# Optimization experiments

Measured on AMD Instinct MI355X. Metric: run time of the kernel, lower is better.

The kernel has to match this reference:

```python
import jax, jax.numpy as jnp
import numpy as np

B, N, C, K = 8, 4096, 128, 16
EPS = 1e-5  # BatchNorm1d default eps


def setup_inputs() -> dict:
    key = jax.random.key(0)
    k0, k1, k2 = jax.random.split(key, 3)
    xyz = jax.random.normal(k0, (B, N, 3), jnp.float32)
    x = jax.random.normal(k1, (B, C, N), jnp.float32)
    # Conv1d(channel, channel, kernel_size=1, bias=False) weight -> [C_out, C_in]
    W = jax.random.normal(k2, (C, C), jnp.float32) / np.sqrt(C)
    gamma = jnp.ones((C,), jnp.float32)
    beta = jnp.zeros((C,), jnp.float32)
    running_mean = jnp.zeros((C,), jnp.float32)
    running_var = jnp.ones((C,), jnp.float32)
    return {"xyz": xyz, "x": x, "W": W, "gamma": gamma, "beta": beta,
            "running_mean": running_mean, "running_var": running_var}


def _knn_idx(xyz, k):
    # squared pairwise distances d2[b,i,j] = ||xyz[b,i]-xyz[b,j]||^2
    s = jnp.sum(xyz * xyz, axis=-1)                      # [B,N]
    d2 = s[:, :, None] + s[:, None, :] - 2.0 * jnp.einsum('bnd,bmd->bnm', xyz, xyz)
    # keops argKmin over dim=1; d2 is symmetric so top_k over the last axis is equivalent
    _, idx = jax.lax.top_k(-d2, k)                       # [B,N,K]
    return idx


def reference(xyz, x, W, gamma, beta, running_mean, running_var):
    idx = _knn_idx(xyz, K)                               # [B,N,K] int32
    x_t = jnp.transpose(x, (0, 2, 1))                    # [B,N,C]
    grouped = jax.vmap(lambda pts, i: pts[i])(x_t, idx)  # [B,N,K,C] gather
    g = jnp.transpose(grouped, (0, 3, 2, 1))             # [B,C,K,N]
    # 1x1 Conv1d (no bias): GEMM over channel dim
    y = jnp.einsum('oc,bckn->bokn', W, g)                # [B,C,K,N]
    # BatchNorm1d (inference form with running stats)
    scale = gamma * jax.lax.rsqrt(running_var + EPS)     # [C]
    y = y * scale[None, :, None, None] + (beta - running_mean * scale)[None, :, None, None]
    y = jax.nn.relu(y)
    return jnp.max(y, axis=2)                            # max over k neighbors -> [B,C,N]
```

## Files before the change

kernel.cpp:

```cpp
#include <hip/hip_runtime.h>
#include <hip/hip_bf16.h>

#define BATCH 8
#define NPTS  4096
#define CCH   128
#define KNN_K 16

typedef __attribute__((ext_vector_type(8))) short  bf16x8;
typedef __attribute__((ext_vector_type(4))) float  f32x4;


static __device__ __forceinline__ short f2bf(float v) {
    __hip_bfloat16 h = __float2bfloat16(v);
    return __builtin_bit_cast(short, h);
}

__global__ __launch_bounds__(256) void transpose_kernel(
    const float* __restrict__ x, short* __restrict__ xTb)
{
    __shared__ short tile[64 * 66];
    const int tid = threadIdx.x;
    const int b   = blockIdx.x >> 7;
    const int rem = blockIdx.x & 127;
    const int nt  = rem >> 1;
    const int ct  = rem & 1;

    #pragma unroll
    for (int it = 0; it < 16; ++it) {
        const int idx = it * 256 + tid;
        const int cc  = idx >> 6;
        const int nn  = idx & 63;
        const float v = x[(size_t)(b * CCH + ct * 64 + cc) * NPTS + nt * 64 + nn];
        tile[cc * 66 + nn] = f2bf(v);
    }
    __syncthreads();
    #pragma unroll
    for (int it = 0; it < 16; ++it) {
        const int idx = it * 256 + tid;
        const int nn  = idx >> 6;
        const int cc  = idx & 63;
        xTb[(size_t)(b * NPTS + nt * 64 + nn) * CCH + ct * 64 + cc] = tile[cc * 66 + nn];
    }
}

__global__ __launch_bounds__(256) void small_prep_kernel(
    const float* __restrict__ xyz, const float* __restrict__ W,
    const float* __restrict__ gamma, const float* __restrict__ beta,
    const float* __restrict__ rmean, const float* __restrict__ rvar,
    short* __restrict__ Wb, float* __restrict__ scale, float* __restrict__ bias,
    float4* __restrict__ pts)
{
    const int t = blockIdx.x * 256 + threadIdx.x;
    if (t < CCH * CCH) Wb[t] = f2bf(W[t]);
    if (t < CCH) {
        const float s = gamma[t] / sqrtf(rvar[t] + 1e-5f);
        scale[t] = s;
        bias[t]  = beta[t] - rmean[t] * s;
    }
    {
        #pragma clang fp contract(off)
        const float px = xyz[3 * t + 0];
        const float py = xyz[3 * t + 1];
        const float pz = xyz[3 * t + 2];
        const float s  = px * px + py * py + pz * pz;
        pts[t] = make_float4(px, py, pz, s);
    }
}

#define PK_(h, l) ((((unsigned long long)(h)) << 32) | (unsigned long long)(l))

static __device__ __forceinline__ void knn_body(
    const int bid, const int tid,
    const float4* __restrict__ pts, unsigned short* __restrict__ knn)
{
    const int lane = tid & 63;
    const int wid  = tid >> 6;
    const int g    = lane >> 4;
    const int s    = lane & 15;
    const int wq   = bid * 16 + wid * 4;
    const int b    = wq >> 12;
    const int i    = (wq & 4095) + g;
    const float4* pb = pts + (b << 12);

    const float4 q = pb[i];

    const unsigned SENT_HI = 0xFF7FFFFFu;
    const unsigned SENT_LO = 0xFFFFFFFFu;

    unsigned lhi = SENT_HI, llo = SENT_LO;
    float bufD = 0.f;
    int   bufJ = 0;
    int   cnt  = 0;
    float tau  = 3.4e38f;
    const int gsh = g << 4;

    auto sort16 = [&](unsigned& hi, unsigned& lo) {
        #define CE_(K, J, OFF) { \
            const unsigned ohi = (unsigned)__builtin_amdgcn_ds_swizzle((int)hi, OFF); \
            const unsigned olo = (unsigned)__builtin_amdgcn_ds_swizzle((int)lo, OFF); \
            const bool olt = PK_(ohi, olo) < PK_(hi, lo); \
            const bool sel = (((s & (J)) == 0) == ((s & (K)) == 0)); \
            const bool tk  = sel ? olt : !olt; \
            hi = tk ? ohi : hi; lo = tk ? olo : lo; }
        CE_(2, 1, 0x041F)
        CE_(4, 2, 0x081F)  CE_(4, 1, 0x041F)
        CE_(8, 4, 0x101F)  CE_(8, 2, 0x081F)  CE_(8, 1, 0x041F)
        CE_(16, 8, 0x201F) CE_(16, 4, 0x101F) CE_(16, 2, 0x081F) CE_(16, 1, 0x041F)
        #undef CE_
    };

    auto refresh_tau = [&]() {
        const unsigned thi = (unsigned)__builtin_amdgcn_ds_swizzle((int)lhi, 0x01F0);
        tau = __uint_as_float((thi & 0x80000000u) ? (thi & 0x7FFFFFFFu) : ~thi);
    };

    auto flush = [&]() {
        const unsigned u = __float_as_uint(bufD);
        unsigned khi = (u & 0x80000000u) ? ~u : (u | 0x80000000u);
        unsigned klo = (unsigned)bufJ;
        const bool inval = (s >= cnt);
        khi = inval ? SENT_HI : khi;
        klo = inval ? SENT_LO : klo;
        sort16(khi, klo);
        {
            const unsigned rhi = (unsigned)__builtin_amdgcn_ds_swizzle((int)khi, 0x3C1F);
            const unsigned rlo = (unsigned)__builtin_amdgcn_ds_swizzle((int)klo, 0x3C1F);
            const bool rlt = PK_(rhi, rlo) < PK_(lhi, llo);
            lhi = rlt ? rhi : lhi; llo = rlt ? rlo : llo;
        }
        #define MC_(J, OFF) { \
            const unsigned ohi = (unsigned)__builtin_amdgcn_ds_swizzle((int)lhi, OFF); \
            const unsigned olo = (unsigned)__builtin_amdgcn_ds_swizzle((int)llo, OFF); \
            const bool olt = PK_(ohi, olo) < PK_(lhi, llo); \
            const bool tk  = ((s & (J)) == 0) ? olt : !olt; \
            lhi = tk ? ohi : lhi; llo = tk ? olo : llo; }
        MC_(8, 0x201F) MC_(4, 0x101F) MC_(2, 0x081F) MC_(1, 0x041F)
        #undef MC_
        refresh_tau();
        cnt = 0;
    };

    #define SUB_(DD, C, JB) { \
        const unsigned long long mask = __ballot((DD) < tau); \
        if (mask) { \
            const unsigned sub = (unsigned)((mask >> gsh) & 0xFFFFull); \
            const int m = __popc(sub); \
            if (__any(cnt + m > 15)) flush(); \
            const bool surv = (sub >> s) & 1u; \
            const int rank  = __popc(sub & ((1u << s) - 1u)); \
            const int dest  = surv ? (cnt + rank) : 15;    \
            const int addr  = (gsh | dest) << 2; \
            const int nd = __builtin_amdgcn_ds_permute(addr, __float_as_int(DD)); \
            const int nj = __builtin_amdgcn_ds_permute(addr, (JB) + ((C) << 4) + s); \
            const bool got = (s >= cnt) & (s < cnt + m); \
            bufD = got ? __int_as_float(nd) : bufD; \
            bufJ = got ? nj : bufJ; \
            cnt += m; \
        } }

    auto process = [&](const float4& p0, const float4& p1,
                       const float4& p2, const float4& p3, const int jbase) {
        float dd0, dd1, dd2, dd3;
        {
            #pragma clang fp contract(off)
            dd0 = (q.w + p0.w) - 2.0f * (q.x * p0.x + q.y * p0.y + q.z * p0.z);
            dd1 = (q.w + p1.w) - 2.0f * (q.x * p1.x + q.y * p1.y + q.z * p1.z);
            dd2 = (q.w + p2.w) - 2.0f * (q.x * p2.x + q.y * p2.y + q.z * p2.z);
            dd3 = (q.w + p3.w) - 2.0f * (q.x * p3.x + q.y * p3.y + q.z * p3.z);
        }
        SUB_(dd0, 0, jbase)
        SUB_(dd1, 1, jbase)
        SUB_(dd2, 2, jbase)
        SUB_(dd3, 3, jbase)
    };

    const float4* lp = pb + s;
    float4 a0 = lp[0],  a1 = lp[16],  a2 = lp[32],  a3 = lp[48];
    float4 c0 = lp[64], c1 = lp[80],  c2 = lp[96],  c3 = lp[112];

    {
        float dd0, dd1, dd2, dd3;
        {
            #pragma clang fp contract(off)
            dd0 = (q.w + a0.w) - 2.0f * (q.x * a0.x + q.y * a0.y + q.z * a0.z);
            dd1 = (q.w + a1.w) - 2.0f * (q.x * a1.x + q.y * a1.y + q.z * a1.z);
            dd2 = (q.w + a2.w) - 2.0f * (q.x * a2.x + q.y * a2.y + q.z * a2.z);
            dd3 = (q.w + a3.w) - 2.0f * (q.x * a3.x + q.y * a3.y + q.z * a3.z);
        }
        const unsigned u = __float_as_uint(dd0);
        lhi = (u & 0x80000000u) ? ~u : (u | 0x80000000u);
        llo = (unsigned)s;
        sort16(lhi, llo);
        refresh_tau();
        SUB_(dd1, 1, 0)
        SUB_(dd2, 2, 0)
        SUB_(dd3, 3, 0)
    }

    #pragma unroll 1
    for (int t = 0; t < 31; ++t) {
        const int blk = 1 + 2 * t;
        const float4* p2 = lp + (blk + 1) * 64;
        a0 = p2[0]; a1 = p2[16]; a2 = p2[32]; a3 = p2[48];
        process(c0, c1, c2, c3, blk * 64);
        const float4* p3 = lp + (blk + 2) * 64;
        c0 = p3[0]; c1 = p3[16]; c2 = p3[32]; c3 = p3[48];
        process(a0, a1, a2, a3, (blk + 1) * 64);
    }
    process(c0, c1, c2, c3, 63 * 64);
    #undef SUB_

    flush();

    unsigned short* o = knn + ((((size_t)b << 12) + i) << 4);
    o[s] = (unsigned short)llo;
}

static __device__ __forceinline__ void zgemm_body(
    const int bid, const int tid,
    const short* __restrict__ xTb, const short* __restrict__ Wb,
    short* __restrict__ Zb)
{
    const int lane = tid & 63;
    const int wid  = tid >> 6;
    const int kl   = lane & 15;
    const int q8   = (lane >> 4) * 8;

    const int    G    = bid * 64 + wid * 16 + kl;
    const size_t arow = (size_t)G * CCH;

    const f32x4 zero = {0.f, 0.f, 0.f, 0.f};
    f32x4 acc[8];
    #pragma unroll
    for (int t = 0; t < 8; ++t) acc[t] = zero;

    #pragma unroll 1
    for (int kk = 0; kk < 4; ++kk) {
        const bf16x8 a = *(const bf16x8*)(xTb + arow + kk * 32 + q8);
        #pragma unroll 2
        for (int t = 0; t < 8; ++t) {
            const bf16x8 bf = *(const bf16x8*)(Wb + (t * 16 + kl) * CCH + kk * 32 + q8);
            acc[t] = __builtin_amdgcn_mfma_f32_16x16x32_bf16(a, bf, acc[t], 0, 0, 0);
        }
    }

    const int rbase = bid * 64 + wid * 16 + (lane >> 4) * 4;
    #pragma unroll
    for (int t = 0; t < 8; ++t)
        #pragma unroll
        for (int r = 0; r < 4; ++r)
            Zb[(size_t)(rbase + r) * CCH + t * 16 + kl] = f2bf(acc[t][r]);
}

__global__ __launch_bounds__(256, 8) void knn_zgemm_kernel(
    const float4* __restrict__ pts, unsigned short* __restrict__ knn,
    const short* __restrict__ xTb, const short* __restrict__ Wb,
    short* __restrict__ Zb)
{
    const int bid = blockIdx.x;
    const int qd  = bid / 5;
    const int rm  = bid - qd * 5;
    if (rm == 4) {
        zgemm_body(qd, threadIdx.x, xTb, Wb, Zb);
    } else {
        knn_body(qd * 4 + rm, threadIdx.x, pts, knn);
    }
}

__global__ __launch_bounds__(256) void gmax_kernel(
    const short* __restrict__ Zb, const unsigned short* __restrict__ knn,
    const float* __restrict__ scale, const float* __restrict__ bias,
    float* __restrict__ out)
{
    __shared__ float sm[16][132];
    const int lane = threadIdx.x & 63;
    const int wid  = threadIdx.x >> 6;
    const int n0   = blockIdx.x * 16;
    const int b    = blockIdx.x >> 8;
    const float s0 = scale[2 * lane],   s1 = scale[2 * lane + 1];
    const float t0 = bias[2 * lane],    t1 = bias[2 * lane + 1];

    for (int p = 0; p < 4; ++p) {
        const int n = n0 + wid * 4 + p;
        const unsigned short* kr = knn + (size_t)n * 16;
        float m0 = 0.f, m1 = 0.f;
        #pragma unroll
        for (int k = 0; k < 16; ++k) {
            const int r = (int)kr[k];
            const unsigned v = *(const unsigned*)(Zb + ((size_t)(b * NPTS + r)) * CCH + 2 * lane);
            const float z0 = __uint_as_float(v << 16);
            const float z1 = __uint_as_float(v & 0xFFFF0000u);
            m0 = fmaxf(m0, s0 * z0 + t0);
            m1 = fmaxf(m1, s1 * z1 + t1);
        }
        sm[wid * 4 + p][2 * lane]     = m0;
        sm[wid * 4 + p][2 * lane + 1] = m1;
    }
    __syncthreads();

    const int c    = threadIdx.x & 127;
    const int half = threadIdx.x >> 7;
    float v[8];
    #pragma unroll
    for (int i = 0; i < 8; ++i) v[i] = sm[half * 8 + i][c];
    float4 f0 = {v[0], v[1], v[2], v[3]};
    float4 f1 = {v[4], v[5], v[6], v[7]};
    float* op = out + ((size_t)(b * CCH + c)) * NPTS + (n0 & 4095) + half * 8;
    *(float4*)op       = f0;
    *(float4*)(op + 4) = f1;
}

extern "C" void kernel_launch(void* const* d_in, const int* in_sizes, int n_in,
                              void* d_out, int out_size, void* d_ws, size_t ws_size,
                              hipStream_t stream)
{
    const float* xyz   = (const float*)d_in[0];
    const float* x     = (const float*)d_in[1];
    const float* W     = (const float*)d_in[2];
    const float* gamma = (const float*)d_in[3];
    const float* beta  = (const float*)d_in[4];
    const float* rmean = (const float*)d_in[5];
    const float* rvar  = (const float*)d_in[6];
    float* out = (float*)d_out;

    char* ws = (char*)d_ws;
    short*          xTb   = (short*)(ws);
    short*          Wb    = (short*)(ws + 8388608);
    float*          scale = (float*)(ws + 8421376);
    float*          bias  = (float*)(ws + 8421888);
    float4*         pts   = (float4*)(ws + 8422400);
    unsigned short* knn   = (unsigned short*)(ws + 8946688);
    short*          Zb    = (short*)(ws + 9995264);

    transpose_kernel<<<BATCH * 64 * 2, 256, 0, stream>>>(x, xTb);
    small_prep_kernel<<<BATCH * NPTS / 256, 256, 0, stream>>>(
        xyz, W, gamma, beta, rmean, rvar, Wb, scale, bias, pts);
    knn_zgemm_kernel<<<BATCH * NPTS / 16 + BATCH * NPTS / 64, 256, 0, stream>>>(
        pts, knn, xTb, Wb, Zb);
    gmax_kernel<<<BATCH * NPTS / 16, 256, 0, stream>>>(Zb, knn, scale, bias, out);
}
```

Baseline: 120.6 us.

## Split fused knn/zgemm kernel into separate launches and stage W in LDS

Splits the combined kNN+GEMM kernel, which interleaved block roles, into two separate kernels launched one after the other on the same stream. The GEMM kernel now loads the bf16 weight matrix into padded shared memory and fully unrolls its loops, replacing repeated global reads of W. This removes the overlap that the fused launch allowed between compute-heavy kNN and memory-heavy GEMM blocks. In exchange it adds a launch and the GEMM can no longer hide behind the kNN work. The knn kernel also loses its occupancy hint of 8 blocks in launch_bounds.

Measured after the change: 112.9 us. -6.4%, faster.

```diff
diff --git a/kernel.cpp b/kernel.cpp
--- a/kernel.cpp
+++ b/kernel.cpp
@@ -69,15 +69,14 @@
 
 #define PK_(h, l) ((((unsigned long long)(h)) << 32) | (unsigned long long)(l))
 
-static __device__ __forceinline__ void knn_body(
-    const int bid, const int tid,
+__global__ __launch_bounds__(256) void knn_kernel(
     const float4* __restrict__ pts, unsigned short* __restrict__ knn)
 {
-    const int lane = tid & 63;
-    const int wid  = tid >> 6;
+    const int lane = threadIdx.x & 63;
+    const int wid  = threadIdx.x >> 6;
     const int g    = lane >> 4;
     const int s    = lane & 15;
-    const int wq   = bid * 16 + wid * 4;
+    const int wq   = blockIdx.x * 16 + wid * 4;
     const int b    = wq >> 12;
     const int i    = (wq & 4095) + g;
     const float4* pb = pts + (b << 12);
@@ -216,55 +215,48 @@
     o[s] = (unsigned short)llo;
 }
 
-static __device__ __forceinline__ void zgemm_body(
-    const int bid, const int tid,
+__global__ __launch_bounds__(256) void zgemm_kernel(
     const short* __restrict__ xTb, const short* __restrict__ Wb,
     short* __restrict__ Zb)
 {
-    const int lane = tid & 63;
-    const int wid  = tid >> 6;
+    __shared__ short sW[CCH * 136];
+    const int lane = threadIdx.x & 63;
+    const int wid  = threadIdx.x >> 6;
     const int kl   = lane & 15;
     const int q8   = (lane >> 4) * 8;
 
-    const int    G    = bid * 64 + wid * 16 + kl;
+    #pragma unroll
+    for (int it = 0; it < 8; ++it) {
+        const int e = (it * 256 + threadIdx.x) * 8;
+        const int r = e >> 7, c = e & 127;
+        *(bf16x8*)(sW + r * 136 + c) = *(const bf16x8*)(Wb + e);
+    }
+
+    const int    G    = blockIdx.x * 64 + wid * 16 + kl;
     const size_t arow = (size_t)G * CCH;
+    __syncthreads();
 
     const f32x4 zero = {0.f, 0.f, 0.f, 0.f};
     f32x4 acc[8];
     #pragma unroll
     for (int t = 0; t < 8; ++t) acc[t] = zero;
 
-    #pragma unroll 1
+    #pragma unroll
     for (int kk = 0; kk < 4; ++kk) {
         const bf16x8 a = *(const bf16x8*)(xTb + arow + kk * 32 + q8);
-        #pragma unroll 2
+        #pragma unroll
         for (int t = 0; t < 8; ++t) {
-            const bf16x8 bf = *(const bf16x8*)(Wb + (t * 16 + kl) * CCH + kk * 32 + q8);
+            const bf16x8 bf = *(const bf16x8*)(sW + (t * 16 + kl) * 136 + kk * 32 + q8);
             acc[t] = __builtin_amdgcn_mfma_f32_16x16x32_bf16(a, bf, acc[t], 0, 0, 0);
         }
     }
 
-    const int rbase = bid * 64 + wid * 16 + (lane >> 4) * 4;
+    const int rbase = blockIdx.x * 64 + wid * 16 + (lane >> 4) * 4;
     #pragma unroll
     for (int t = 0; t < 8; ++t)
         #pragma unroll
         for (int r = 0; r < 4; ++r)
             Zb[(size_t)(rbase + r) * CCH + t * 16 + kl] = f2bf(acc[t][r]);
-}
-
-__global__ __launch_bounds__(256, 8) void knn_zgemm_kernel(
-    const float4* __restrict__ pts, unsigned short* __restrict__ knn,
-    const short* __restrict__ xTb, const short* __restrict__ Wb,
-    short* __restrict__ Zb)
-{
-    const int bid = blockIdx.x;
-    const int qd  = bid / 5;
-    const int rm  = bid - qd * 5;
-    if (rm == 4) {
-        zgemm_body(qd, threadIdx.x, xTb, Wb, Zb);
-    } else {
-        knn_body(qd * 4 + rm, threadIdx.x, pts, knn);
-    }
 }
 
 __global__ __launch_bounds__(256) void gmax_kernel(
@@ -335,7 +327,7 @@
     transpose_kernel<<<BATCH * 64 * 2, 256, 0, stream>>>(x, xTb);
     small_prep_kernel<<<BATCH * NPTS / 256, 256, 0, stream>>>(
         xyz, W, gamma, beta, rmean, rvar, Wb, scale, bias, pts);
-    knn_zgemm_kernel<<<BATCH * NPTS / 16 + BATCH * NPTS / 64, 256, 0, stream>>>(
-        pts, knn, xTb, Wb, Zb);
+    knn_kernel<<<BATCH * NPTS / 16, 256, 0, stream>>>(pts, knn);
+    zgemm_kernel<<<BATCH * NPTS / 64, 256, 0, stream>>>(xTb, Wb, Zb);
     gmax_kernel<<<BATCH * NPTS / 16, 256, 0, stream>>>(Zb, knn, scale, bias, out);
 }
```
